# Kernel optimization log

Hardware: AMD Instinct MI355X
Metric: run time of the kernel (lower is better)

Reference implementation:

```python
import jax, jax.numpy as jnp
import numpy as np

N_NODES = 20000
N_EDGES = 320000
N_FEAT = 128
N_CLASS = 10
NEG_SLOPE = 0.2  # PyG GATConv default LeakyReLU slope


def gat_conv(x, src, dst, ew, W, a_src, a_dst, b, heads, ch, concat):
    """PyG-style GATConv with multiplicative edge_weight on messages.
    x: [N, Fin]; src/dst: [E] (self-loops already included); ew: [E].
    """
    N = x.shape[0]
    h = (x @ W).reshape(N, heads, ch)                      # [N,H,C]
    al_s = jnp.sum(h * a_src, axis=-1)                     # [N,H]
    al_d = jnp.sum(h * a_dst, axis=-1)                     # [N,H]
    e = jax.nn.leaky_relu(al_s[src] + al_d[dst], NEG_SLOPE)  # [E,H]
    # segment softmax over incoming edges of each target node
    m = jax.ops.segment_max(e, dst, num_segments=N)        # [N,H]
    ex = jnp.exp(e - m[dst])
    den = jax.ops.segment_sum(ex, dst, num_segments=N)     # [N,H]
    alpha = ex / (den[dst] + 1e-16)                        # [E,H]
    msg = h[src] * (alpha * ew[:, None])[..., None]        # [E,H,C]
    out = jax.ops.segment_sum(msg, dst, num_segments=N)    # [N,H,C]
    out = out.reshape(N, heads * ch) if concat else out.mean(axis=1)
    return out + b


def setup_inputs() -> dict:
    key = jax.random.key(0)
    ks = jax.random.split(key, 20)
    d = {}
    d["x"] = jax.random.normal(ks[0], (N_NODES, N_FEAT), dtype=jnp.float32)
    d["edge_index"] = jax.random.randint(ks[1], (2, N_EDGES), 0, N_NODES, dtype=jnp.int32)
    d["edge_weight"] = jnp.ones((N_EDGES,), dtype=jnp.float32)

    def glorot(k, shape):
        fan = shape[0] + shape[-1]
        return jax.random.uniform(k, shape, jnp.float32, -1.0, 1.0) * np.sqrt(6.0 / fan)

    H1, C1 = 4, 256
    H3, C3 = 6, N_CLASS
    d["W1"] = glorot(ks[2], (N_FEAT, H1 * C1))
    d["a1s"] = glorot(ks[3], (H1, C1)) * 0.1
    d["a1d"] = glorot(ks[4], (H1, C1)) * 0.1
    d["b1"] = jnp.zeros((H1 * C1,), jnp.float32)
    d["lw1"] = glorot(ks[5], (N_FEAT, H1 * C1))
    d["lb1"] = jnp.zeros((H1 * C1,), jnp.float32)

    d["W2"] = glorot(ks[6], (H1 * C1, H1 * C1))
    d["a2s"] = glorot(ks[7], (H1, C1)) * 0.1
    d["a2d"] = glorot(ks[8], (H1, C1)) * 0.1
    d["b2"] = jnp.zeros((H1 * C1,), jnp.float32)
    d["lw2"] = glorot(ks[9], (H1 * C1, H1 * C1))
    d["lb2"] = jnp.zeros((H1 * C1,), jnp.float32)

    d["W3"] = glorot(ks[10], (H1 * C1, H3 * C3))
    d["a3s"] = glorot(ks[11], (H3, C3)) * 0.1
    d["a3d"] = glorot(ks[12], (H3, C3)) * 0.1
    d["b3"] = jnp.zeros((C3,), jnp.float32)
    d["lw3"] = glorot(ks[13], (H1 * C1, C3))
    d["lb3"] = jnp.zeros((C3,), jnp.float32)
    return d


def reference(x, edge_index, edge_weight,
              W1, a1s, a1d, b1, lw1, lb1,
              W2, a2s, a2d, b2, lw2, lb2,
              W3, a3s, a3d, b3, lw3, lb3):
    N = x.shape[0]
    # PyG GATConv adds self-loops (fill edge_weight with 1.0)
    loop = jnp.arange(N, dtype=edge_index.dtype)
    src = jnp.concatenate([edge_index[0], loop])
    dst = jnp.concatenate([edge_index[1], loop])
    ew = jnp.concatenate([edge_weight, jnp.ones((N,), edge_weight.dtype)])

    h = jax.nn.elu(gat_conv(x, src, dst, ew, W1, a1s, a1d, b1, 4, 256, True)
                   + (x @ lw1 + lb1))
    h = jax.nn.elu(gat_conv(h, src, dst, ew, W2, a2s, a2d, b2, 4, 256, True)
                   + (h @ lw2 + lb2))
    out = gat_conv(h, src, dst, ew, W3, a3s, a3d, b3, 6, N_CLASS, False) \
          + (h @ lw3 + lb3)
    return out
```

## Files before the change

### kernel.cpp

```cpp
#include <hip/hip_runtime.h>

typedef __attribute__((ext_vector_type(8))) short s16x8;
typedef __attribute__((ext_vector_type(8))) __bf16 bf16x8;
typedef __attribute__((ext_vector_type(4))) float f32x4;

__device__ inline float bf2f(ushort u){ return __uint_as_float(((unsigned)u)<<16); }
__device__ inline ushort f2bf(float f){
  unsigned u = __float_as_uint(f);
  unsigned r = (u + 0x7fffu + ((u>>16)&1u)) >> 16;
  return (ushort)r;
}

__device__ inline void gl_lds16(const ushort* g, ushort* l){
  __builtin_amdgcn_global_load_lds(
      (const __attribute__((address_space(1))) unsigned int*)g,
      (__attribute__((address_space(3))) unsigned int*)l,
      16, 0, 0);
}

__global__ void k_count(const int* __restrict__ ei, int* __restrict__ counts,
                        int E, int ET){
  int e = blockIdx.x*256 + threadIdx.x;
  if (e >= ET) return;
  int dst = (e < E) ? ei[E + e] : (e - E);
  atomicAdd(&counts[dst], 1);
}

__global__ __launch_bounds__(1024) void k_scan(const int* __restrict__ cnt,
                                               int* __restrict__ indptr, int N){
  __shared__ int part[1024];
  int t = threadIdx.x;
  int per = (N + 1023) / 1024;
  int base = t * per;
  int s = 0;
  for (int i = 0; i < per; ++i){ int idx = base + i; if (idx < N) s += cnt[idx]; }
  part[t] = s; __syncthreads();
  for (int off = 1; off < 1024; off <<= 1){
    int v = (t >= off) ? part[t-off] : 0;
    __syncthreads();
    if (t >= off) part[t] += v;
    __syncthreads();
  }
  int run = (t == 0) ? 0 : part[t-1];
  for (int i = 0; i < per; ++i){
    int idx = base + i;
    if (idx < N){ indptr[idx] = run; run += cnt[idx]; }
  }
  if (t == 1023) indptr[N] = run;
}

__global__ void k_fill(const int* __restrict__ ei, const float* __restrict__ ew,
                       const int* __restrict__ indptr, int* __restrict__ cursor,
                       int* __restrict__ csrc, float* __restrict__ cew,
                       int E, int ET){
  int e = blockIdx.x*256 + threadIdx.x;
  if (e >= ET) return;
  int src, dst; float w;
  if (e < E){ src = ei[e]; dst = ei[E + e]; w = ew[e]; }
  else { src = dst = e - E; w = 1.0f; }
  int pos = indptr[dst] + atomicAdd(&cursor[dst], 1);
  csrc[pos] = src; cew[pos] = w;
}

__global__ void k_f2b(const float* __restrict__ x, ushort* __restrict__ xb,
                      int n8valid, int n8total){
  int i = blockIdx.x*256 + threadIdx.x;
  if (i >= n8total) return;
  s16x8 o = {0,0,0,0,0,0,0,0};
  if (i < n8valid){
    const float4* p = (const float4*)x + (size_t)i*2;
    float4 a = p[0], b = p[1];
    o[0]=(short)f2bf(a.x); o[1]=(short)f2bf(a.y); o[2]=(short)f2bf(a.z); o[3]=(short)f2bf(a.w);
    o[4]=(short)f2bf(b.x); o[5]=(short)f2bf(b.y); o[6]=(short)f2bf(b.z); o[7]=(short)f2bf(b.w);
  }
  *((s16x8*)xb + i) = o;
}

__global__ __launch_bounds__(256) void k_packB(
    const float* __restrict__ W, const float* __restrict__ LW,
    ushort* __restrict__ BT, int K, int NW, int NL, int Npad)
{
  __shared__ float tile[32][33];
  int k0 = blockIdx.x*32, n0 = blockIdx.y*32;
  int c = threadIdx.x & 31, r4 = threadIdx.x >> 5;
  #pragma unroll
  for (int rr = 0; rr < 32; rr += 8){
    int k = k0 + r4 + rr, n = n0 + c;
    float v = 0.f;
    if (k < K){
      if (n < NW)            v = W[(size_t)k*NW + n];
      else if (n < NW + NL)  v = LW[(size_t)k*NL + (n - NW)];
    }
    tile[r4+rr][c] = v;
  }
  __syncthreads();
  #pragma unroll
  for (int rr = 0; rr < 32; rr += 8){
    int n = n0 + r4 + rr, k = k0 + c;
    if (n < Npad && k < K) BT[(size_t)n*K + k] = f2bf(tile[c][r4+rr]);
  }
}

__global__ __launch_bounds__(256) void k_gemm(
    const ushort* __restrict__ A, const ushort* __restrict__ BT,
    ushort* __restrict__ Gatt, ushort* __restrict__ Skip,
    int K, int GW, int SW, int NCB, int CPX)
{
  __shared__ ushort As[128*64];
  __shared__ ushort Bs[128*64];
  const int bid = blockIdx.x;
  const int lb = CPX ? ((bid & 7)*CPX + (bid >> 3)) : bid;
  const size_t row0 = (size_t)(lb / NCB) * 128;
  const size_t col0 = (size_t)(lb % NCB) * 128;
  const int t = threadIdx.x;
  const int l = t & 63, w = t >> 6;
  const int wr = w >> 1, wc = w & 1;
  const int sr = l >> 3;
  const int sk = ((l & 7) ^ sr) << 3;
  const ushort* gA = A  + (row0 + w*8 + sr)*(size_t)K + sk;
  const ushort* gB = BT + (col0 + w*8 + sr)*(size_t)K + sk;
  ushort* lA = As + w*512;
  ushort* lB = Bs + w*512;
  const int rf = l & 15;
  const int g4 = l >> 4;
  f32x4 acc[4][4] = {};

  for (int k0 = 0; k0 < K; k0 += 64){
    #pragma unroll
    for (int i = 0; i < 4; ++i){
      gl_lds16(gA + k0 + (size_t)(i*32)*K, lA + i*2048);
      gl_lds16(gB + k0 + (size_t)(i*32)*K, lB + i*2048);
    }
    __syncthreads();
    #pragma unroll
    for (int kk = 0; kk < 2; ++kk){
      const int koff = ((((kk<<2) | g4) ^ (rf & 7)) << 3);
      bf16x8 af[4], bfr[4];
      #pragma unroll
      for (int i = 0; i < 4; ++i)
        af[i] = __builtin_bit_cast(bf16x8, *(const s16x8*)(As + (wr*64 + i*16 + rf)*64 + koff));
      #pragma unroll
      for (int j = 0; j < 4; ++j)
        bfr[j] = __builtin_bit_cast(bf16x8, *(const s16x8*)(Bs + (wc*64 + j*16 + rf)*64 + koff));
      #pragma unroll
      for (int i = 0; i < 4; ++i)
        #pragma unroll
        for (int j = 0; j < 4; ++j)
          acc[i][j] = __builtin_amdgcn_mfma_f32_16x16x32_bf16(af[i], bfr[j], acc[i][j], 0, 0, 0);
    }
    __syncthreads();
  }

  #pragma unroll
  for (int i = 0; i < 4; ++i){
    #pragma unroll
    for (int j = 0; j < 4; ++j){
      int gc = (int)col0 + wc*64 + j*16 + rf;
      #pragma unroll
      for (int r = 0; r < 4; ++r){
        size_t gr = row0 + wr*64 + i*16 + (g4<<2) + r;
        float v = acc[i][j][r];
        if (gc < GW)            Gatt[gr*GW + gc] = f2bf(v);
        else if (gc < GW + SW)  Skip[gr*SW + (gc - GW)] = f2bf(v);
      }
    }
  }
}

#define STG8(p0, hh, ktv, offU) do { \
  const ushort* _g = (p0) + (((size_t)(hh))<<7)*(size_t)K + (((size_t)(ktv))<<6); \
  gl_lds16(_g, S + (offU) + (w<<9)); \
  gl_lds16(_g + ((size_t)K<<6), S + (offU) + 4096 + (w<<9)); \
} while(0)

#define RD_A(base_) do { _Pragma("unroll") \
  for (int i_ = 0; i_ < 4; ++i_){ \
    const int hr = wr*64 + i_*16 + rf; const int sw = hr & 7; \
    av[i_][0] = *(const bf16x8*)((base_) + hr*64 + ((g4 ^ sw) << 3)); \
    av[i_][1] = *(const bf16x8*)((base_) + hr*64 + (((4|g4) ^ sw) << 3)); } \
} while(0)

#define RD_B(base_, dst_) do { _Pragma("unroll") \
  for (int j_ = 0; j_ < 2; ++j_){ \
    const int cf = wc*32 + j_*16 + rf; const int sw = cf & 7; \
    dst_[j_][0] = *(const bf16x8*)((base_) + cf*64 + ((g4 ^ sw) << 3)); \
    dst_[j_][1] = *(const bf16x8*)((base_) + cf*64 + (((4|g4) ^ sw) << 3)); } \
} while(0)

#define MM8(mh, nh, bv_) do { \
  asm volatile("s_barrier" ::: "memory"); \
  __builtin_amdgcn_s_setprio(1); \
  _Pragma("unroll") \
  for (int kk_ = 0; kk_ < 2; ++kk_) \
    _Pragma("unroll") \
    for (int i_ = 0; i_ < 4; ++i_) \
      _Pragma("unroll") \
      for (int j_ = 0; j_ < 2; ++j_) \
        acc[mh][nh][i_][j_] = __builtin_amdgcn_mfma_f32_16x16x32_bf16( \
            av[i_][kk_], bv_[j_][kk_], acc[mh][nh][i_][j_], 0, 0, 0); \
  __builtin_amdgcn_s_setprio(0); \
} while(0)

__global__ __launch_bounds__(512, 1) void k_gemm8(
    const ushort* __restrict__ A, const ushort* __restrict__ BT,
    ushort* __restrict__ Gatt, ushort* __restrict__ Skip,
    int K, int GW, int CPX)
{
  __shared__ ushort S[65536];
  const int bid = blockIdx.x;
  const int lb = (bid & 7)*CPX + (bid >> 3);
  const size_t row0 = (size_t)(lb >> 3) * 256;
  const size_t col0 = (size_t)(lb & 7) * 256;
  const int t = threadIdx.x;
  const int l = t & 63, w = t >> 6;
  const int wr = w >> 2, wc = w & 3;
  const int rf = l & 15, g4 = l >> 4;
  const int T = K >> 6;

  const int r0 = t >> 3, s0 = t & 7;
  const ushort* pA = A  + (row0 + r0)*(size_t)K + ((s0 ^ (r0 & 7)) << 3);
  const ushort* pB = BT + (col0 + r0)*(size_t)K + ((s0 ^ (r0 & 7)) << 3);

  f32x4 acc[2][2][4][2] = {};
  bf16x8 av[4][2], bvlo[2][2], bvhi[2][2];

  STG8(pA, 0, 0, 0);
  STG8(pB, 0, 0, 16384);
  STG8(pA, 1, 0, 8192);
  STG8(pB, 1, 0, 24576);
  STG8(pA, 0, 1, 32768);
  STG8(pB, 0, 1, 49152);
  asm volatile("s_waitcnt vmcnt(4)");
  asm volatile("s_barrier" ::: "memory");

  for (int u = 0; u < T; ++u){
    const int b = u & 1;
    const int bbase = b << 15;
    const int nbase = bbase ^ 32768;
    const bool un1 = (u + 1 < T), un2 = (u + 2 < T);
    const ushort* Alo = S + bbase;
    const ushort* Ahi = S + bbase + 8192;
    const ushort* Blo = S + bbase + 16384;
    const ushort* Bhi = S + bbase + 24576;
    RD_A(Alo); RD_B(Blo, bvlo);
    if (un1) STG8(pA, 1, u+1, nbase + 8192);
    MM8(0, 0, bvlo);
    asm volatile("s_barrier" ::: "memory");
    RD_B(Bhi, bvhi);
    if (un1) STG8(pB, 1, u+1, nbase + 24576);
    MM8(0, 1, bvhi);
    asm volatile("s_barrier" ::: "memory");
    RD_A(Ahi);
    if (un2) STG8(pA, 0, u+2, bbase);
    MM8(1, 1, bvhi);
    asm volatile("s_barrier" ::: "memory");
    if (un2) STG8(pB, 0, u+2, bbase + 16384);
    MM8(1, 0, bvlo);
    if (un2) asm volatile("s_waitcnt vmcnt(4)");
    else     asm volatile("s_waitcnt vmcnt(0)");
    asm volatile("s_barrier" ::: "memory");
  }

  ushort* outp; int cb;
  if ((int)col0 < GW){ outp = Gatt; cb = (int)col0; }
  else               { outp = Skip; cb = (int)col0 - GW; }
  #pragma unroll
  for (int mh = 0; mh < 2; ++mh)
    #pragma unroll
    for (int i = 0; i < 4; ++i)
      #pragma unroll
      for (int rr = 0; rr < 4; ++rr){
        size_t gr = row0 + mh*128 + wr*64 + i*16 + (g4<<2) + rr;
        ushort* rp = outp + gr*1024 + cb;
        #pragma unroll
        for (int nh = 0; nh < 2; ++nh)
          #pragma unroll
          for (int j = 0; j < 2; ++j)
            rp[nh*128 + wc*32 + j*16 + rf] = f2bf(acc[mh][nh][i][j][rr]);
      }
}

__global__ __launch_bounds__(256) void k_al(const ushort* __restrict__ Gatt,
    const float* __restrict__ a_s, const float* __restrict__ a_d,
    float* __restrict__ als, float* __restrict__ ald, int N){
  int gw = (blockIdx.x*blockDim.x + threadIdx.x) >> 6;
  int l = threadIdx.x & 63;
  if (gw >= N) return;
  const ushort* row = Gatt + (size_t)gw*1024;
  int c0 = l*16;
  s16x8 v0 = *(const s16x8*)(row + c0);
  s16x8 v1 = *(const s16x8*)(row + c0 + 8);
  float ps = 0.f, pd = 0.f;
  #pragma unroll
  for (int q = 0; q < 8; ++q){
    float f0 = bf2f((ushort)v0[q]), f1 = bf2f((ushort)v1[q]);
    ps += f0*a_s[c0+q] + f1*a_s[c0+8+q];
    pd += f0*a_d[c0+q] + f1*a_d[c0+8+q];
  }
  #pragma unroll
  for (int off = 8; off; off >>= 1){
    ps += __shfl_down(ps, off);
    pd += __shfl_down(pd, off);
  }
  if ((l & 15) == 0){
    als[(size_t)gw*4 + (l>>4)] = ps;
    ald[(size_t)gw*4 + (l>>4)] = pd;
  }
}

__global__ __launch_bounds__(256) void k_agg(
    const ushort* __restrict__ Gatt,
    const ushort* __restrict__ Skip,
    const float*  __restrict__ als,
    const float*  __restrict__ ald,
    const float*  __restrict__ bias,
    const float*  __restrict__ lbias,
    const int*    __restrict__ indptr,
    const int*    __restrict__ csrc,
    const float*  __restrict__ cew,
    ushort* __restrict__ Hout,
    int N)
{
  const int n = blockIdx.x;
  const int t = threadIdx.x;
  if (n >= N){
    ushort4 z = {0,0,0,0};
    *(ushort4*)(Hout + (size_t)n*1024 + t*4) = z;
    return;
  }
  const int l = t & 63, w = t >> 6;
  const int beg = indptr[n];
  const int deg = indptr[n+1] - beg;
  __shared__ float s_ald[4], s_m[4], s_den[4];
  __shared__ int   s_src[64];
  __shared__ float s_w[64][4];
  __shared__ float s_part[3][64][16];
  if (t < 4) s_ald[t] = ald[(size_t)n*4 + t];
  __syncthreads();
  const bool fast = (deg <= 64);

  if (fast){
    int e2 = t >> 2, hh = t & 3;
    if (e2 < deg){
      int s = csrc[beg + e2];
      if (hh == 0) s_src[e2] = s;
      float r_ = als[(size_t)s*4 + hh] + s_ald[hh];
      s_w[e2][hh] = r_ > 0.f ? r_ : 0.2f*r_;
    }
    __syncthreads();
    float mye = (l < deg) ? s_w[l][w] : -1e30f;
    float mx = mye;
    #pragma unroll
    for (int o = 32; o; o >>= 1) mx = fmaxf(mx, __shfl_xor(mx, o));
    float ex = (l < deg) ? __expf(mye - mx) : 0.f;
    float den = ex;
    #pragma unroll
    for (int o = 32; o; o >>= 1) den += __shfl_xor(den, o);
    den += 1e-16f;
    if (l < deg) s_w[l][w] = ex / den * cew[beg + l];
    __syncthreads();
  } else {
    const float aldh = s_ald[w];
    float mx = -1e30f;
    for (int i = l; i < deg; i += 64){
      int s = csrc[beg+i];
      float e = als[(size_t)s*4 + w] + aldh;
      e = e > 0.f ? e : 0.2f*e;
      mx = fmaxf(mx, e);
    }
    #pragma unroll
    for (int off = 32; off; off >>= 1) mx = fmaxf(mx, __shfl_xor(mx, off));
    if (l == 0) s_m[w] = mx;
    __syncthreads();
    const float mh = s_m[w];
    float den = 0.f;
    for (int i = l; i < deg; i += 64){
      int s = csrc[beg+i];
      float e = als[(size_t)s*4 + w] + aldh;
      e = e > 0.f ? e : 0.2f*e;
      den += __expf(e - mh);
    }
    #pragma unroll
    for (int off = 32; off; off >>= 1) den += __shfl_xor(den, off);
    if (l == 0) s_den[w] = den + 1e-16f;
    __syncthreads();
  }

  const int h2 = l >> 4;
  const ushort* gbase = Gatt + (size_t)l*16;
  float a[16];
  #pragma unroll
  for (int q = 0; q < 16; ++q) a[q] = 0.f;
  for (int c0 = 0; c0 < deg; c0 += 64){
    int nc = min(64, deg - c0);
    if (!fast){
      int ei2 = t >> 2, hh = t & 3;
      if (ei2 < nc){
        int s = csrc[beg + c0 + ei2];
        if (hh == 0) s_src[ei2] = s;
        float e = als[(size_t)s*4 + hh] + s_ald[hh];
        e = e > 0.f ? e : 0.2f*e;
        s_w[ei2][hh] = __expf(e - s_m[hh]) / s_den[hh] * cew[beg + c0 + ei2];
      }
      __syncthreads();
    }
    for (int j = w; j < nc; j += 4){
      int s = s_src[j];
      float wg = s_w[j][h2];
      const ushort* rp = gbase + (size_t)s*1024;
      s16x8 h0 = *(const s16x8*)rp;
      s16x8 h1 = *(const s16x8*)(rp + 8);
      #pragma unroll
      for (int q = 0; q < 8; ++q) a[q] += wg * bf2f((ushort)h0[q]);
      #pragma unroll
      for (int q = 0; q < 8; ++q) a[q+8] += wg * bf2f((ushort)h1[q]);
    }
    __syncthreads();
  }
  if (w){
    #pragma unroll
    for (int q = 0; q < 16; ++q) s_part[w-1][l][q] = a[q];
  }
  __syncthreads();
  if (w == 0){
    #pragma unroll
    for (int q = 0; q < 16; ++q) a[q] += s_part[0][l][q] + s_part[1][l][q] + s_part[2][l][q];
    const int col = l*16;
    s16x8 sk0 = *(const s16x8*)(Skip + (size_t)n*1024 + col);
    s16x8 sk1 = *(const s16x8*)(Skip + (size_t)n*1024 + col + 8);
    s16x8 ov0, ov1;
    #pragma unroll
    for (int q = 0; q < 8; ++q){
      float v = a[q] + bias[col+q] + lbias[col+q] + bf2f((ushort)sk0[q]);
      v = v > 0.f ? v : __expf(v) - 1.f;
      ov0[q] = (short)f2bf(v);
      float v2 = a[q+8] + bias[col+8+q] + lbias[col+8+q] + bf2f((ushort)sk1[q]);
      v2 = v2 > 0.f ? v2 : __expf(v2) - 1.f;
      ov1[q] = (short)f2bf(v2);
    }
    *(s16x8*)(Hout + (size_t)n*1024 + col)     = ov0;
    *(s16x8*)(Hout + (size_t)n*1024 + col + 8) = ov1;
  }
}

__global__ void k_al3(const ushort* __restrict__ G3, const float* __restrict__ a_s,
                      const float* __restrict__ a_d,
                      float* __restrict__ als, float* __restrict__ ald, int N){
  int n = blockIdx.x*256 + threadIdx.x;
  if (n >= N) return;
  const ushort* row = G3 + (size_t)n*60;
  #pragma unroll
  for (int h = 0; h < 6; ++h){
    float ps = 0.f, pd = 0.f;
    #pragma unroll
    for (int c = 0; c < 10; ++c){
      float v = bf2f(row[h*10 + c]);
      ps += v * a_s[h*10 + c];
      pd += v * a_d[h*10 + c];
    }
    als[(size_t)n*6 + h] = ps;
    ald[(size_t)n*6 + h] = pd;
  }
}

__global__ __launch_bounds__(64) void k_agg3(
    const ushort* __restrict__ G3,
    const ushort* __restrict__ Skip3,
    const float*  __restrict__ als,
    const float*  __restrict__ ald,
    const float*  __restrict__ b3,
    const float*  __restrict__ lb3,
    const int*    __restrict__ indptr,
    const int*    __restrict__ csrc,
    const float*  __restrict__ cew,
    float* __restrict__ out, int N)
{
  const int n = blockIdx.x;
  const int l = threadIdx.x;
  const int beg = indptr[n], deg = indptr[n+1] - beg;
  __shared__ float s_aldh[6];
  __shared__ int   s_src[64];
  __shared__ float s_wgt[64][6];
  __shared__ float s_o[6][10];
  if (l < 6) s_aldh[l] = ald[(size_t)n*6 + l];
  __syncthreads();
  float m0=-1e30f,m1=-1e30f,m2=-1e30f,m3=-1e30f,m4=-1e30f,m5=-1e30f;
  float d0=0.f,d1=0.f,d2=0.f,d3=0.f,d4=0.f,d5=0.f;
  for (int c0 = 0; c0 < deg; c0 += 64){
    int nc = min(64, deg - c0);
    bool act = l < nc;
    int s = act ? csrc[beg + c0 + l] : 0;
#define HP(hh, mm, dd) { \
    float e = -1e30f; \
    if (act){ float r_ = als[(size_t)s*6 + hh] + s_aldh[hh]; e = r_ > 0.f ? r_ : 0.2f*r_; } \
    float cm = e; \
    for (int o_ = 32; o_; o_ >>= 1) cm = fmaxf(cm, __shfl_xor(cm, o_)); \
    float nm = fmaxf(mm, cm); \
    float ex = act ? __expf(e - nm) : 0.f; \
    for (int o_ = 32; o_; o_ >>= 1) ex += __shfl_xor(ex, o_); \
    dd = dd * __expf(mm - nm) + ex; mm = nm; }
    HP(0,m0,d0) HP(1,m1,d1) HP(2,m2,d2) HP(3,m3,d3) HP(4,m4,d4) HP(5,m5,d5)
#undef HP
  }
  const int h = l / 10, c = l % 10;
  float o = 0.f;
  for (int c0 = 0; c0 < deg; c0 += 64){
    int nc = min(64, deg - c0);
    if (l < nc){
      int s = csrc[beg + c0 + l];
      s_src[l] = s;
      float w_ = cew[beg + c0 + l];
#define WP(hh, mm, dd) { \
      float r_ = als[(size_t)s*6 + hh] + s_aldh[hh]; \
      float e = r_ > 0.f ? r_ : 0.2f*r_; \
      s_wgt[l][hh] = __expf(e - mm) / (dd + 1e-16f) * w_; }
      WP(0,m0,d0) WP(1,m1,d1) WP(2,m2,d2) WP(3,m3,d3) WP(4,m4,d4) WP(5,m5,d5)
#undef WP
    }
    __syncthreads();
    if (l < 60){
      for (int i = 0; i < nc; ++i)
        o += s_wgt[i][h] * bf2f(G3[(size_t)s_src[i]*60 + l]);
    }
    __syncthreads();
  }
  if (l < 60) s_o[h][c] = o;
  __syncthreads();
  if (l < 10){
    float v = (s_o[0][l]+s_o[1][l]+s_o[2][l]+s_o[3][l]+s_o[4][l]+s_o[5][l]) * (1.0f/6.0f);
    v += b3[l] + lb3[l] + bf2f(Skip3[(size_t)n*10 + l]);
    out[(size_t)n*10 + l] = v;
  }
}

extern "C" void kernel_launch(void* const* d_in, const int* in_sizes, int n_in,
                              void* d_out, int out_size, void* d_ws, size_t ws_size,
                              hipStream_t stream)
{
  const int N = 20000, F = 128, E = 320000, ET = E + N;
  const int Mpad = 20224;
  const int F1 = 1024, NT = 2048;
  const int NWG1 = (Mpad/128)*(NT/128);
  const int NWG2 = (Mpad/256)*(NT/256);

  const float* x   = (const float*)d_in[0];
  const int*   ei  = (const int*)  d_in[1];
  const float* ew  = (const float*)d_in[2];
  const float* W1  = (const float*)d_in[3];
  const float* a1s = (const float*)d_in[4];
  const float* a1d = (const float*)d_in[5];
  const float* b1  = (const float*)d_in[6];
  const float* lw1 = (const float*)d_in[7];
  const float* lb1 = (const float*)d_in[8];
  const float* W2  = (const float*)d_in[9];
  const float* a2s = (const float*)d_in[10];
  const float* a2d = (const float*)d_in[11];
  const float* b2  = (const float*)d_in[12];
  const float* lw2 = (const float*)d_in[13];
  const float* lb2 = (const float*)d_in[14];
  const float* W3  = (const float*)d_in[15];
  const float* a3s = (const float*)d_in[16];
  const float* a3d = (const float*)d_in[17];
  const float* b3  = (const float*)d_in[18];
  const float* lw3 = (const float*)d_in[19];
  const float* lb3 = (const float*)d_in[20];

  char* ws = (char*)d_ws;
  size_t off = 0;
  auto alloc = [&](size_t bytes) -> void* {
    void* p = ws + off;
    off = (off + bytes + 255) & ~(size_t)255;
    return p;
  };
  ushort* Gatt = (ushort*)alloc((size_t)Mpad*F1*2);
  ushort* Skip = (ushort*)alloc((size_t)Mpad*F1*2);
  ushort* H    = (ushort*)alloc((size_t)Mpad*F1*2);
  ushort* xb   = (ushort*)alloc((size_t)Mpad*F*2);
  ushort* BT   = (ushort*)alloc((size_t)NT*1024*2);
  float*  als  = (float*) alloc((size_t)N*6*4);
  float*  ald  = (float*) alloc((size_t)N*6*4);
  int*    counts = (int*)alloc((size_t)2*N*4);
  int*    cursor = counts + N;
  int*    indptr = (int*)alloc((size_t)(N+1)*4);
  int*    csrc   = (int*)alloc((size_t)ET*4);
  float*  cew    = (float*)alloc((size_t)ET*4);
  if (off > ws_size) return;

  hipMemsetAsync(counts, 0, (size_t)2*N*4, stream);
  k_count<<<(ET+255)/256, 256, 0, stream>>>(ei, counts, E, ET);
  k_scan<<<1, 1024, 0, stream>>>(counts, indptr, N);
  k_fill<<<(ET+255)/256, 256, 0, stream>>>(ei, ew, indptr, cursor, csrc, cew, E, ET);
  k_f2b<<<(Mpad*F/8+255)/256, 256, 0, stream>>>(x, xb, N*F/8, Mpad*F/8);

  k_packB<<<dim3((F+31)/32, NT/32), 256, 0, stream>>>(W1, lw1, BT, F, 1024, 1024, NT);
  k_gemm<<<dim3(NWG1), 256, 0, stream>>>(xb, BT, Gatt, Skip, F, 1024, 1024, NT/128, NWG1/8);
  k_al<<<(N+3)/4, 256, 0, stream>>>(Gatt, a1s, a1d, als, ald, N);
  k_agg<<<Mpad, 256, 0, stream>>>(Gatt, Skip, als, ald, b1, lb1, indptr, csrc, cew, H, N);

  k_packB<<<dim3(F1/32, NT/32), 256, 0, stream>>>(W2, lw2, BT, F1, 1024, 1024, NT);
  k_gemm8<<<dim3(NWG2), 512, 0, stream>>>(H, BT, Gatt, Skip, F1, 1024, NWG2/8);
  k_al<<<(N+3)/4, 256, 0, stream>>>(Gatt, a2s, a2d, als, ald, N);
  k_agg<<<Mpad, 256, 0, stream>>>(Gatt, Skip, als, ald, b2, lb2, indptr, csrc, cew, H, N);

  k_packB<<<dim3(F1/32, 128/32), 256, 0, stream>>>(W3, lw3, BT, F1, 60, 10, 128);
  k_gemm<<<dim3(Mpad/128), 256, 0, stream>>>(H, BT, Gatt, Skip, F1, 60, 10, 1, 0);
  k_al3<<<(N+255)/256, 256, 0, stream>>>(Gatt, a3s, a3d, als, ald, N);
  k_agg3<<<N, 64, 0, stream>>>(Gatt, Skip, als, ald, b3, lb3, indptr, csrc, cew,
                               (float*)d_out, N);
}
```

Baseline: 503.9 us.

## Switch 8-wave GEMM to 32x32x16 bf16 MFMA with hoisted B fragment reads

Replaces the 16x16x32 MFMA tiling in the 8-wave GEMM with 32x32x16 MFMAs, reworking the LDS fragment reads, accumulator layout and epilogue store mapping to match. Both B halves are now read up front, and the barrier inside the MFMA macro is dropped, so there are fewer LDS reads per flop and fewer barriers per k-step. The trade-off is higher register pressure from the larger B fragments held live, and a possible change in LDS bank-conflict behaviour with the new swizzle indexing.

```diff
diff --git a/kernel.cpp b/kernel.cpp
--- a/kernel.cpp
+++ b/kernel.cpp
@@ -3,6 +3,7 @@
 typedef __attribute__((ext_vector_type(8))) short s16x8;
 typedef __attribute__((ext_vector_type(8))) __bf16 bf16x8;
 typedef __attribute__((ext_vector_type(4))) float f32x4;
+typedef __attribute__((ext_vector_type(16))) float f32x16;
 
 __device__ inline float bf2f(ushort u){ return __uint_as_float(((unsigned)u)<<16); }
 __device__ inline ushort f2bf(float f){
@@ -173,31 +174,29 @@
   gl_lds16(_g + ((size_t)K<<6), S + (offU) + 4096 + (w<<9)); \
 } while(0)
 
-#define RD_A(base_) do { _Pragma("unroll") \
-  for (int i_ = 0; i_ < 4; ++i_){ \
-    const int hr = wr*64 + i_*16 + rf; const int sw = hr & 7; \
-    av[i_][0] = *(const bf16x8*)((base_) + hr*64 + ((g4 ^ sw) << 3)); \
-    av[i_][1] = *(const bf16x8*)((base_) + hr*64 + (((4|g4) ^ sw) << 3)); } \
+#define RD_A32(base_) do { _Pragma("unroll") \
+  for (int rt_ = 0; rt_ < 2; ++rt_){ \
+    const ushort* rp_ = (base_) + (wr*64 + rt_*32 + l31)*64; \
+    _Pragma("unroll") \
+    for (int kk_ = 0; kk_ < 4; ++kk_) \
+      av[rt_][kk_] = *(const bf16x8*)(rp_ + ((((kk_<<1) | g2) ^ sw_) << 3)); } \
 } while(0)
 
-#define RD_B(base_, dst_) do { _Pragma("unroll") \
-  for (int j_ = 0; j_ < 2; ++j_){ \
-    const int cf = wc*32 + j_*16 + rf; const int sw = cf & 7; \
-    dst_[j_][0] = *(const bf16x8*)((base_) + cf*64 + ((g4 ^ sw) << 3)); \
-    dst_[j_][1] = *(const bf16x8*)((base_) + cf*64 + (((4|g4) ^ sw) << 3)); } \
+#define RD_B32(base_, dst_) do { \
+  const ushort* rp_ = (base_) + (wc*32 + l31)*64; \
+  _Pragma("unroll") \
+  for (int kk_ = 0; kk_ < 4; ++kk_) \
+    dst_[kk_] = *(const bf16x8*)(rp_ + ((((kk_<<1) | g2) ^ sw_) << 3)); \
 } while(0)
 
-#define MM8(mh, nh, bv_) do { \
-  asm volatile("s_barrier" ::: "memory"); \
+#define MM32(mh, nh, bv_) do { \
   __builtin_amdgcn_s_setprio(1); \
   _Pragma("unroll") \
-  for (int kk_ = 0; kk_ < 2; ++kk_) \
+  for (int kk_ = 0; kk_ < 4; ++kk_) \
     _Pragma("unroll") \
-    for (int i_ = 0; i_ < 4; ++i_) \
-      _Pragma("unroll") \
-      for (int j_ = 0; j_ < 2; ++j_) \
-        acc[mh][nh][i_][j_] = __builtin_amdgcn_mfma_f32_16x16x32_bf16( \
-            av[i_][kk_], bv_[j_][kk_], acc[mh][nh][i_][j_], 0, 0, 0); \
+    for (int rt_ = 0; rt_ < 2; ++rt_) \
+      acc[mh][nh][rt_] = __builtin_amdgcn_mfma_f32_32x32x16_bf16( \
+          av[rt_][kk_], bv_[kk_], acc[mh][nh][rt_], 0, 0, 0); \
   __builtin_amdgcn_s_setprio(0); \
 } while(0)
 
@@ -214,15 +213,16 @@
   const int t = threadIdx.x;
   const int l = t & 63, w = t >> 6;
   const int wr = w >> 2, wc = w & 3;
-  const int rf = l & 15, g4 = l >> 4;
+  const int l31 = l & 31, g2 = l >> 5;
+  const int sw_ = l31 & 7;
   const int T = K >> 6;
 
   const int r0 = t >> 3, s0 = t & 7;
   const ushort* pA = A  + (row0 + r0)*(size_t)K + ((s0 ^ (r0 & 7)) << 3);
   const ushort* pB = BT + (col0 + r0)*(size_t)K + ((s0 ^ (r0 & 7)) << 3);
 
-  f32x4 acc[2][2][4][2] = {};
-  bf16x8 av[4][2], bvlo[2][2], bvhi[2][2];
+  f32x16 acc[2][2][2] = {};
+  bf16x8 av[2][4], bvlo[4], bvhi[4];
 
   STG8(pA, 0, 0, 0);
   STG8(pB, 0, 0, 16384);
@@ -242,20 +242,19 @@
     const ushort* Ahi = S + bbase + 8192;
     const ushort* Blo = S + bbase + 16384;
     const ushort* Bhi = S + bbase + 24576;
-    RD_A(Alo); RD_B(Blo, bvlo);
+    RD_A32(Alo); RD_B32(Blo, bvlo); RD_B32(Bhi, bvhi);
     if (un1) STG8(pA, 1, u+1, nbase + 8192);
-    MM8(0, 0, bvlo);
+    MM32(0, 0, bvlo);
     asm volatile("s_barrier" ::: "memory");
-    RD_B(Bhi, bvhi);
     if (un1) STG8(pB, 1, u+1, nbase + 24576);
-    MM8(0, 1, bvhi);
+    MM32(0, 1, bvhi);
     asm volatile("s_barrier" ::: "memory");
-    RD_A(Ahi);
+    RD_A32(Ahi);
     if (un2) STG8(pA, 0, u+2, bbase);
-    MM8(1, 1, bvhi);
+    MM32(1, 0, bvlo);
     asm volatile("s_barrier" ::: "memory");
     if (un2) STG8(pB, 0, u+2, bbase + 16384);
-    MM8(1, 0, bvlo);
+    MM32(1, 1, bvhi);
     if (un2) asm volatile("s_waitcnt vmcnt(4)");
     else     asm volatile("s_waitcnt vmcnt(0)");
     asm volatile("s_barrier" ::: "memory");
@@ -267,16 +266,14 @@
   #pragma unroll
   for (int mh = 0; mh < 2; ++mh)
     #pragma unroll
-    for (int i = 0; i < 4; ++i)
+    for (int rt = 0; rt < 2; ++rt)
       #pragma unroll
-      for (int rr = 0; rr < 4; ++rr){
-        size_t gr = row0 + mh*128 + wr*64 + i*16 + (g4<<2) + rr;
+      for (int r = 0; r < 16; ++r){
+        size_t gr = row0 + mh*128 + wr*64 + rt*32 + (r&3) + ((r>>2)<<3) + (g2<<2);
         ushort* rp = outp + gr*1024 + cb;
         #pragma unroll
         for (int nh = 0; nh < 2; ++nh)
-          #pragma unroll
-          for (int j = 0; j < 2; ++j)
-            rp[nh*128 + wc*32 + j*16 + rf] = f2bf(acc[mh][nh][i][j][rr]);
+          rp[nh*128 + wc*32 + l31] = f2bf(acc[mh][nh][rt][r]);
       }
 }
 
```

After: 502.3 us. Within noise of the previous version (-0.3%).

## Assign one wavefront per node in GAT aggregation with online softmax

Applied to the files above, without the earlier changes.

The aggregation kernel now gives each node a single 64-lane wavefront instead of a 256-thread block. It computes the segment softmax with an online max/sum pass over 16-edge chunks and broadcasts edge weights and source indices with shuffles. This removes shared memory, block barriers and the cross-wave partial-sum reduction, at the cost of less parallelism per node for high-degree nodes. Separately, an s_barrier is dropped from the MFMA macro in the second-layer GEMM, which could risk LDS races if that barrier was needed.

```diff
diff --git a/kernel.cpp b/kernel.cpp
--- a/kernel.cpp
+++ b/kernel.cpp
@@ -188,7 +188,6 @@
 } while(0)
 
 #define MM8(mh, nh, bv_) do { \
-  asm volatile("s_barrier" ::: "memory"); \
   __builtin_amdgcn_s_setprio(1); \
   _Pragma("unroll") \
   for (int kk_ = 0; kk_ < 2; ++kk_) \
@@ -321,126 +320,86 @@
     ushort* __restrict__ Hout,
     int N)
 {
-  const int n = blockIdx.x;
   const int t = threadIdx.x;
+  const int l = t & 63, w = t >> 6;
+  const int n = blockIdx.x*4 + w;
+  const int h2 = l >> 4;
+  const int col = l*16;
   if (n >= N){
-    ushort4 z = {0,0,0,0};
-    *(ushort4*)(Hout + (size_t)n*1024 + t*4) = z;
+    s16x8 z = {0,0,0,0,0,0,0,0};
+    *(s16x8*)(Hout + (size_t)n*1024 + col)     = z;
+    *(s16x8*)(Hout + (size_t)n*1024 + col + 8) = z;
     return;
   }
-  const int l = t & 63, w = t >> 6;
   const int beg = indptr[n];
   const int deg = indptr[n+1] - beg;
-  __shared__ float s_ald[4], s_m[4], s_den[4];
-  __shared__ int   s_src[64];
-  __shared__ float s_w[64][4];
-  __shared__ float s_part[3][64][16];
-  if (t < 4) s_ald[t] = ald[(size_t)n*4 + t];
-  __syncthreads();
-  const bool fast = (deg <= 64);
-
-  if (fast){
-    int e2 = t >> 2, hh = t & 3;
-    if (e2 < deg){
-      int s = csrc[beg + e2];
-      if (hh == 0) s_src[e2] = s;
-      float r_ = als[(size_t)s*4 + hh] + s_ald[hh];
-      s_w[e2][hh] = r_ > 0.f ? r_ : 0.2f*r_;
-    }
-    __syncthreads();
-    float mye = (l < deg) ? s_w[l][w] : -1e30f;
-    float mx = mye;
-    #pragma unroll
-    for (int o = 32; o; o >>= 1) mx = fmaxf(mx, __shfl_xor(mx, o));
-    float ex = (l < deg) ? __expf(mye - mx) : 0.f;
-    float den = ex;
-    #pragma unroll
-    for (int o = 32; o; o >>= 1) den += __shfl_xor(den, o);
-    den += 1e-16f;
-    if (l < deg) s_w[l][w] = ex / den * cew[beg + l];
-    __syncthreads();
-  } else {
-    const float aldh = s_ald[w];
-    float mx = -1e30f;
-    for (int i = l; i < deg; i += 64){
-      int s = csrc[beg+i];
-      float e = als[(size_t)s*4 + w] + aldh;
-      e = e > 0.f ? e : 0.2f*e;
-      mx = fmaxf(mx, e);
-    }
-    #pragma unroll
-    for (int off = 32; off; off >>= 1) mx = fmaxf(mx, __shfl_xor(mx, off));
-    if (l == 0) s_m[w] = mx;
-    __syncthreads();
-    const float mh = s_m[w];
-    float den = 0.f;
-    for (int i = l; i < deg; i += 64){
-      int s = csrc[beg+i];
-      float e = als[(size_t)s*4 + w] + aldh;
-      e = e > 0.f ? e : 0.2f*e;
-      den += __expf(e - mh);
-    }
-    #pragma unroll
-    for (int off = 32; off; off >>= 1) den += __shfl_xor(den, off);
-    if (l == 0) s_den[w] = den + 1e-16f;
-    __syncthreads();
-  }
-
-  const int h2 = l >> 4;
-  const ushort* gbase = Gatt + (size_t)l*16;
+  const int hh = l & 3;
+  const float aldh = ald[(size_t)n*4 + hh];
+
+  float m = -1e30f, d = 0.f;
+  for (int c0 = 0; c0 < deg; c0 += 16){
+    int i = c0 + (l >> 2);
+    bool act = (i < deg);
+    float e = -1e30f;
+    if (act){
+      int s = csrc[beg + i];
+      float r_ = als[(size_t)s*4 + hh] + aldh;
+      e = r_ > 0.f ? r_ : 0.2f*r_;
+    }
+    float cm = e;
+    #pragma unroll
+    for (int o = 4; o < 64; o <<= 1) cm = fmaxf(cm, __shfl_xor(cm, o));
+    float nm = fmaxf(m, cm);
+    float ex = act ? __expf(e - nm) : 0.f;
+    #pragma unroll
+    for (int o = 4; o < 64; o <<= 1) ex += __shfl_xor(ex, o);
+    d = d * __expf(m - nm) + ex;
+    m = nm;
+  }
+  d += 1e-16f;
+  const float inv_d = 1.0f / d;
+
   float a[16];
   #pragma unroll
   for (int q = 0; q < 16; ++q) a[q] = 0.f;
-  for (int c0 = 0; c0 < deg; c0 += 64){
-    int nc = min(64, deg - c0);
-    if (!fast){
-      int ei2 = t >> 2, hh = t & 3;
-      if (ei2 < nc){
-        int s = csrc[beg + c0 + ei2];
-        if (hh == 0) s_src[ei2] = s;
-        float e = als[(size_t)s*4 + hh] + s_ald[hh];
-        e = e > 0.f ? e : 0.2f*e;
-        s_w[ei2][hh] = __expf(e - s_m[hh]) / s_den[hh] * cew[beg + c0 + ei2];
-      }
-      __syncthreads();
-    }
-    for (int j = w; j < nc; j += 4){
-      int s = s_src[j];
-      float wg = s_w[j][h2];
+  const ushort* gbase = Gatt + col;
+  for (int c0 = 0; c0 < deg; c0 += 16){
+    int i = c0 + (l >> 2);
+    int nc = min(16, deg - c0);
+    float wv = 0.f; int sv = 0;
+    if (i < deg){
+      sv = csrc[beg + i];
+      float r_ = als[(size_t)sv*4 + hh] + aldh;
+      float e = r_ > 0.f ? r_ : 0.2f*r_;
+      wv = __expf(e - m) * inv_d * cew[beg + i];
+    }
+    for (int jj = 0; jj < nc; ++jj){
+      float wg = __shfl(wv, (jj << 2) | h2);
+      int s    = __shfl(sv, jj << 2);
       const ushort* rp = gbase + (size_t)s*1024;
       s16x8 h0 = *(const s16x8*)rp;
       s16x8 h1 = *(const s16x8*)(rp + 8);
       #pragma unroll
-      for (int q = 0; q < 8; ++q) a[q] += wg * bf2f((ushort)h0[q]);
+      for (int q = 0; q < 8; ++q) a[q]   += wg * bf2f((ushort)h0[q]);
       #pragma unroll
       for (int q = 0; q < 8; ++q) a[q+8] += wg * bf2f((ushort)h1[q]);
     }
-    __syncthreads();
-  }
-  if (w){
-    #pragma unroll
-    for (int q = 0; q < 16; ++q) s_part[w-1][l][q] = a[q];
-  }
-  __syncthreads();
-  if (w == 0){
-    #pragma unroll
-    for (int q = 0; q < 16; ++q) a[q] += s_part[0][l][q] + s_part[1][l][q] + s_part[2][l][q];
-    const int col = l*16;
-    s16x8 sk0 = *(const s16x8*)(Skip + (size_t)n*1024 + col);
-    s16x8 sk1 = *(const s16x8*)(Skip + (size_t)n*1024 + col + 8);
-    s16x8 ov0, ov1;
-    #pragma unroll
-    for (int q = 0; q < 8; ++q){
-      float v = a[q] + bias[col+q] + lbias[col+q] + bf2f((ushort)sk0[q]);
-      v = v > 0.f ? v : __expf(v) - 1.f;
-      ov0[q] = (short)f2bf(v);
-      float v2 = a[q+8] + bias[col+8+q] + lbias[col+8+q] + bf2f((ushort)sk1[q]);
-      v2 = v2 > 0.f ? v2 : __expf(v2) - 1.f;
-      ov1[q] = (short)f2bf(v2);
-    }
-    *(s16x8*)(Hout + (size_t)n*1024 + col)     = ov0;
-    *(s16x8*)(Hout + (size_t)n*1024 + col + 8) = ov1;
-  }
+  }
+
+  s16x8 sk0 = *(const s16x8*)(Skip + (size_t)n*1024 + col);
+  s16x8 sk1 = *(const s16x8*)(Skip + (size_t)n*1024 + col + 8);
+  s16x8 ov0, ov1;
+  #pragma unroll
+  for (int q = 0; q < 8; ++q){
+    float v = a[q] + bias[col+q] + lbias[col+q] + bf2f((ushort)sk0[q]);
+    v = v > 0.f ? v : __expf(v) - 1.f;
+    ov0[q] = (short)f2bf(v);
+    float v2 = a[q+8] + bias[col+8+q] + lbias[col+8+q] + bf2f((ushort)sk1[q]);
+    v2 = v2 > 0.f ? v2 : __expf(v2) - 1.f;
+    ov1[q] = (short)f2bf(v2);
+  }
+  *(s16x8*)(Hout + (size_t)n*1024 + col)     = ov0;
+  *(s16x8*)(Hout + (size_t)n*1024 + col + 8) = ov1;
 }
 
 __global__ void k_al3(const ushort* __restrict__ G3, const float* __restrict__ a_s,
@@ -595,12 +554,12 @@
   k_packB<<<dim3((F+31)/32, NT/32), 256, 0, stream>>>(W1, lw1, BT, F, 1024, 1024, NT);
   k_gemm<<<dim3(NWG1), 256, 0, stream>>>(xb, BT, Gatt, Skip, F, 1024, 1024, NT/128, NWG1/8);
   k_al<<<(N+3)/4, 256, 0, stream>>>(Gatt, a1s, a1d, als, ald, N);
-  k_agg<<<Mpad, 256, 0, stream>>>(Gatt, Skip, als, ald, b1, lb1, indptr, csrc, cew, H, N);
+  k_agg<<<Mpad/4, 256, 0, stream>>>(Gatt, Skip, als, ald, b1, lb1, indptr, csrc, cew, H, N);
 
   k_packB<<<dim3(F1/32, NT/32), 256, 0, stream>>>(W2, lw2, BT, F1, 1024, 1024, NT);
   k_gemm8<<<dim3(NWG2), 512, 0, stream>>>(H, BT, Gatt, Skip, F1, 1024, NWG2/8);
   k_al<<<(N+3)/4, 256, 0, stream>>>(Gatt, a2s, a2d, als, ald, N);
-  k_agg<<<Mpad, 256, 0, stream>>>(Gatt, Skip, als, ald, b2, lb2, indptr, csrc, cew, H, N);
+  k_agg<<<Mpad/4, 256, 0, stream>>>(Gatt, Skip, als, ald, b2, lb2, indptr, csrc, cew, H, N);
 
   k_packB<<<dim3(F1/32, 128/32), 256, 0, stream>>>(W3, lw3, BT, F1, 60, 10, 128);
   k_gemm<<<dim3(Mpad/128), 256, 0, stream>>>(H, BT, Gatt, Skip, F1, 60, 10, 1, 0);
```

Measured after the change: 501.6 us. About the same (-0.4%).
